# Kernel tuning notes

Hardware: AMD Instinct MI355X
Metric: run time of the kernel (lower is better)

The kernel has to match this reference:

```python
import jax, jax.numpy as jnp
import numpy as np

B, T, C = 2, 2048, 2048
H, HKV, D = 16, 4, 128
THETA = 10000.0
G = H // HKV  # kv groups


def _rope_tables(seq_len, dim, theta):
    inv_freq = 1.0 / theta ** (jnp.arange(0, dim, 2, dtype=jnp.float32) / dim)
    t = jnp.arange(seq_len, dtype=jnp.float32)
    freqs = jnp.outer(t, inv_freq)                 # [T, D/2]
    emb = jnp.concatenate([freqs, freqs], axis=-1)  # [T, D]
    return jnp.cos(emb)[None, None], jnp.sin(emb)[None, None]  # [1,1,T,D]


def _rotate_half(x):
    x1, x2 = jnp.split(x, 2, axis=-1)
    return jnp.concatenate([-x2, x1], axis=-1)


def setup_inputs() -> dict:
    key = jax.random.key(0)
    ks = jax.random.split(key, 6)
    x = jax.random.normal(ks[0], (B, T, C), dtype=jnp.float32)
    s = 0.02
    Wq = jax.random.normal(ks[1], (C, H * D), dtype=jnp.float32) * s
    Wk = jax.random.normal(ks[2], (C, HKV * D), dtype=jnp.float32) * s
    Wv = jax.random.normal(ks[3], (C, HKV * D), dtype=jnp.float32) * s
    Wo = jax.random.normal(ks[4], (H * D, C), dtype=jnp.float32) * s
    mask = jnp.tril(jnp.ones((T, T), dtype=jnp.int32))[None, None]  # causal [1,1,T,T]
    return {"x": x, "Wq": Wq, "Wk": Wk, "Wv": Wv, "Wo": Wo, "mask": mask}


def reference(x, Wq, Wk, Wv, Wo, mask):
    b, t, _ = x.shape
    q = (x @ Wq).reshape(b, t, H, D).transpose(0, 2, 1, 3)      # [B,H,T,D]
    k = (x @ Wk).reshape(b, t, HKV, D).transpose(0, 2, 1, 3)    # [B,HKV,T,D]
    v = (x @ Wv).reshape(b, t, HKV, D).transpose(0, 2, 1, 3)
    cos, sin = _rope_tables(t, D, THETA)
    q = q * cos + _rotate_half(q) * sin
    k = k * cos + _rotate_half(k) * sin
    # expand kv heads (repeat_interleave over head axis)
    k = jnp.repeat(k, G, axis=1)                                # [B,H,T,D]
    v = jnp.repeat(v, G, axis=1)
    attn = jnp.einsum('bhqd,bhkd->bhqk', q, k) / jnp.sqrt(jnp.float32(D))
    attn = jnp.where(mask == 0, jnp.float32(-jnp.inf), attn)
    attn = jax.nn.softmax(attn, axis=-1)
    out = jnp.einsum('bhqk,bhkd->bhqd', attn, v)                # [B,H,T,D]
    out = out.transpose(0, 2, 1, 3).reshape(b, t, H * D)
    return out @ Wo
```

## Files before the change

kernel.cpp:

```cpp
#include <hip/hip_runtime.h>
#include <math.h>

#define B_ 2
#define T_ 2048
#define C_ 2048
#define H_ 16
#define HKV_ 4
#define D_ 128
#define G_ (H_ / HKV_)
#define GK 2048

typedef float f32x4 __attribute__((ext_vector_type(4)));
typedef __bf16 bf16x8 __attribute__((ext_vector_type(8)));

static __device__ __forceinline__ f32x4 mfma16(bf16x8 a, bf16x8 b, f32x4 c) {
    return __builtin_amdgcn_mfma_f32_16x16x32_bf16(a, b, c, 0, 0, 0);
}

static __device__ __forceinline__ void gload16(const __bf16* g, __bf16* l) {
    __builtin_amdgcn_global_load_lds(
        (const __attribute__((address_space(1))) unsigned int*)g,
        (__attribute__((address_space(3))) unsigned int*)l,
        16, 0, 0);
}

__global__ __launch_bounds__(256)
void conv_f32_bf16(const float* __restrict__ src, __bf16* __restrict__ dst, int n8)
{
    const int i = blockIdx.x * blockDim.x + threadIdx.x;
    if (i >= n8) return;
    const float4 a = *(const float4*)&src[(size_t)i * 8];
    const float4 b = *(const float4*)&src[(size_t)i * 8 + 4];
    bf16x8 o;
    o[0] = (__bf16)a.x; o[1] = (__bf16)a.y; o[2] = (__bf16)a.z; o[3] = (__bf16)a.w;
    o[4] = (__bf16)b.x; o[5] = (__bf16)b.y; o[6] = (__bf16)b.z; o[7] = (__bf16)b.w;
    *(bf16x8*)&dst[(size_t)i * 8] = o;
}

__global__ __launch_bounds__(256)
void tconv(const float* __restrict__ src, __bf16* __restrict__ dst, int N)
{
    __shared__ __bf16 tl[32][34];
    const int tx = threadIdx.x;
    const int ty = threadIdx.y;
    const int k0 = blockIdx.x * 32;
    const int n0 = blockIdx.y * 32;

    #pragma unroll
    for (int i = 0; i < 4; ++i) {
        const int r = ty + i * 8;
        tl[r][tx] = (__bf16)src[(size_t)(k0 + r) * N + n0 + tx];
    }
    __syncthreads();
    #pragma unroll
    for (int i = 0; i < 4; ++i) {
        const int r = ty + i * 8;
        dst[(size_t)(n0 + r) * GK + k0 + tx] = tl[tx][r];
    }
}

#define GEMM_MAIN(At, Bt)                                                       \
    __shared__ __bf16 As[128 * 64];                                             \
    __shared__ __bf16 Bs[128 * 64];                                             \
    const int tid = threadIdx.x;                                                \
    const int wave = tid >> 6, lane = tid & 63;                                 \
    const int a = lane & 15, bq = lane >> 4;                                    \
    const int wr = wave >> 1, wc = wave & 1;                                    \
    const int srow = wave * 32 + (lane >> 3);                        \
    const int scol = (lane & 7) * 8;                                            \
    f32x4 acc[4][4];                                                            \
    _Pragma("unroll")                                                           \
    for (int mi = 0; mi < 4; ++mi)                                              \
        _Pragma("unroll")                                                       \
        for (int ni = 0; ni < 4; ++ni) acc[mi][ni] = (f32x4){0.f,0.f,0.f,0.f};  \
    for (int k0 = 0; k0 < GK; k0 += 64) {                                       \
        __syncthreads();                       \
        _Pragma("unroll")                                                       \
        for (int i = 0; i < 4; ++i) {                                           \
            gload16(&(At)[(size_t)(srow + i * 8) * GK + k0 + scol],             \
                    &As[(wave * 32 + i * 8) * 64]);                             \
            gload16(&(Bt)[(size_t)(srow + i * 8) * GK + k0 + scol],             \
                    &Bs[(wave * 32 + i * 8) * 64]);                             \
        }                                                                       \
        __syncthreads();                \
        _Pragma("unroll")                                                       \
        for (int ks = 0; ks < 2; ++ks) {                                        \
            bf16x8 af[4], bfr[4];                                               \
            _Pragma("unroll")                                                   \
            for (int mi = 0; mi < 4; ++mi)                                      \
                af[mi] = *(const bf16x8*)&As[(wr*64 + mi*16 + a) * 64 + ks*32 + bq*8]; \
            _Pragma("unroll")                                                   \
            for (int ni = 0; ni < 4; ++ni)                                      \
                bfr[ni] = *(const bf16x8*)&Bs[(wc*64 + ni*16 + a) * 64 + ks*32 + bq*8]; \
            _Pragma("unroll")                                                   \
            for (int mi = 0; mi < 4; ++mi)                                      \
                _Pragma("unroll")                                               \
                for (int ni = 0; ni < 4; ++ni)                                  \
                    acc[mi][ni] = mfma16(af[mi], bfr[ni], acc[mi][ni]);         \
        }                                                                       \
    }

__global__ __launch_bounds__(256)
void gemm_qkv_mfma(const __bf16* __restrict__ xb,
                   const __bf16* __restrict__ wqt,
                   const __bf16* __restrict__ wkt,
                   const __bf16* __restrict__ wvt,
                   __bf16* __restrict__ qbuf,
                   __bf16* __restrict__ kbuf,
                   __bf16* __restrict__ vbuf)
{
    const int n0 = blockIdx.x * 128;
    const int m0 = blockIdx.y * 128;
    const __bf16* Btp; __bf16* outb; int NH, nloc;
    if (n0 < 2048)      { Btp = wqt + (size_t)n0 * GK;          outb = qbuf; NH = 16; nloc = n0; }
    else if (n0 < 2560) { Btp = wkt + (size_t)(n0 - 2048) * GK; outb = kbuf; NH = 4;  nloc = n0 - 2048; }
    else                { Btp = wvt + (size_t)(n0 - 2560) * GK; outb = vbuf; NH = 4;  nloc = n0 - 2560; }
    const __bf16* Atp = xb + (size_t)m0 * GK;

    GEMM_MAIN(Atp, Btp)

    const int b  = m0 >> 11;
    const int t0 = m0 & (T_ - 1);
    const int h0 = nloc >> 7;
    __bf16* op = outb + (size_t)(b * NH + h0) * T_ * D_;
    #pragma unroll
    for (int mi = 0; mi < 4; ++mi)
        #pragma unroll
        for (int ni = 0; ni < 4; ++ni)
            #pragma unroll
            for (int rr = 0; rr < 4; ++rr) {
                const int row = t0 + wr * 64 + mi * 16 + bq * 4 + rr;
                const int col = wc * 64 + ni * 16 + a;
                op[(size_t)row * D_ + col] = (__bf16)acc[mi][ni][rr];
            }
}

__global__ __launch_bounds__(256)
void gemm_out_mfma(const __bf16* __restrict__ ab,
                   const __bf16* __restrict__ wot,
                   float* __restrict__ outp)
{
    const int n0 = blockIdx.x * 128;
    const int m0 = blockIdx.y * 128;
    const __bf16* Atp = ab + (size_t)m0 * GK;
    const __bf16* Btp = wot + (size_t)n0 * GK;

    GEMM_MAIN(Atp, Btp)

    #pragma unroll
    for (int mi = 0; mi < 4; ++mi)
        #pragma unroll
        for (int ni = 0; ni < 4; ++ni)
            #pragma unroll
            for (int rr = 0; rr < 4; ++rr) {
                const int row = m0 + wr * 64 + mi * 16 + bq * 4 + rr;
                const int col = n0 + wc * 64 + ni * 16 + a;
                outp[(size_t)row * C_ + col] = acc[mi][ni][rr];
            }
}

__global__ void rope_bf16(__bf16* __restrict__ buf)
{
    const int idx = blockIdx.x * blockDim.x + threadIdx.x;
    const int jj  = idx & 31;
    const int row = idx >> 5;
    const int t   = row & (T_ - 1);
    const int d   = jj * 2;

    const float LOG_THETA = 9.210340371976184f;
    const float f1 = (float)t * __expf(-(float)d       * (LOG_THETA / 64.0f));
    const float f2 = (float)t * __expf(-(float)(d + 1) * (LOG_THETA / 64.0f));
    float s1, c1, s2, c2;
    __sincosf(f1, &s1, &c1);
    __sincosf(f2, &s2, &c2);

    __bf16* p = buf + (size_t)row * D_ + d;
    const float x1a = (float)p[0],  x1b = (float)p[1];
    const float x2a = (float)p[64], x2b = (float)p[65];
    p[0]  = (__bf16)(x1a * c1 - x2a * s1);
    p[1]  = (__bf16)(x1b * c2 - x2b * s2);
    p[64] = (__bf16)(x2a * c1 + x1a * s1);
    p[65] = (__bf16)(x2b * c2 + x1b * s2);
}

__global__ __launch_bounds__(256)
void transpose_v(const __bf16* __restrict__ vb, __bf16* __restrict__ vtb)
{
    __shared__ __bf16 tl[32][33];
    const int tx = threadIdx.x;
    const int ty = threadIdx.y;
    const int t0 = blockIdx.x * 32;
    const int d0 = blockIdx.y * 32;
    const int bh = blockIdx.z;

    const __bf16* src = vb + ((size_t)bh * T_ + t0) * D_ + d0;
    #pragma unroll
    for (int i = 0; i < 4; ++i) {
        const int r = ty + i * 8;
        tl[r][tx] = src[(size_t)r * D_ + tx];
    }
    __syncthreads();
    __bf16* dst = vtb + ((size_t)bh * D_ + d0) * T_ + t0;
    #pragma unroll
    for (int i = 0; i < 4; ++i) {
        const int dl = ty + i * 8;
        dst[(size_t)dl * T_ + tx] = tl[tx][dl];
    }
}

#define KS_STRIDE 136
#define VS_STRIDE 36
#define PS_STRIDE 76

__global__ __launch_bounds__(512)
void flash_attn_mfma(const __bf16* __restrict__ qb,
                     const __bf16* __restrict__ kb,
                     const __bf16* __restrict__ vtb,
                     __bf16* __restrict__ abuf)
{
    __shared__ __bf16 KsL[64 * KS_STRIDE];
    __shared__ __bf16 VsL[2 * 128 * VS_STRIDE];
    __shared__ __bf16 PsL[8 * 16 * PS_STRIDE];

    const int tid  = threadIdx.x;
    const int wave = tid >> 6;
    const int lane = tid & 63;
    const int a    = lane & 15;
    const int bq   = lane >> 4;

    const int pair = blockIdx.x;
    const int bh   = blockIdx.y;
    const int b    = bh >> 4;
    const int h    = bh & 15;
    const int kvh  = h >> 2;

    const __bf16* kg  = kb  + (size_t)(b * HKV_ + kvh) * T_ * D_;
    const __bf16* vtg = vtb + (size_t)(b * HKV_ + kvh) * D_ * T_;

    const float scale2 = 0.12750176129424902f;

    for (int half = 0; half < 2; ++half) {
        const int qti = half == 0 ? (15 - pair) : pair;
        const int qt0 = qti * 128;
        const int ntiles = 2 * qti + 2;
        const int qrow_lo = qt0 + wave * 16;

        const __bf16* qg = qb + ((size_t)(b * H_ + h) * T_ + qrow_lo) * D_;
        bf16x8 qf[4];
        #pragma unroll
        for (int ks = 0; ks < 4; ++ks)
            qf[ks] = *(const bf16x8*)&qg[(size_t)a * D_ + ks * 32 + bq * 8];

        f32x4 oacc[8];
        #pragma unroll
        for (int dt = 0; dt < 8; ++dt) oacc[dt] = (f32x4){0.f, 0.f, 0.f, 0.f};
        float m_r[4] = {-INFINITY, -INFINITY, -INFINITY, -INFINITY};
        float l_r[4] = {0.f, 0.f, 0.f, 0.f};

        bf16x8 kpre[2], vpre[2];
        #pragma unroll
        for (int it = 0; it < 2; ++it) {
            const int idx = it * 512 + tid;
            const int r = idx >> 4, c8 = (idx & 15) * 8;
            kpre[it] = *(const bf16x8*)&kg[(size_t)r * D_ + c8];
            const int bo = idx & 3, dd = (idx >> 2) & 127, ss2 = idx >> 9;
            vpre[it] = *(const bf16x8*)&vtg[(size_t)dd * T_ + ss2 * 32 + bo * 8];
        }
        __syncthreads();
        #pragma unroll
        for (int it = 0; it < 2; ++it) {
            const int idx = it * 512 + tid;
            const int r = idx >> 4, c8 = (idx & 15) * 8;
            *(bf16x8*)&KsL[r * KS_STRIDE + c8] = kpre[it];
            const int bo = idx & 3, dd = (idx >> 2) & 127, ss2 = idx >> 9;
            *(bf16x8*)&VsL[(ss2 * 128 + dd) * VS_STRIDE + bo * 8] = vpre[it];
        }
        __syncthreads();

        for (int kt = 0; kt < ntiles; ++kt) {
            const int k0 = kt * 64;
            if (kt + 1 < ntiles) {
                const int k0n = k0 + 64;
                #pragma unroll
                for (int it = 0; it < 2; ++it) {
                    const int idx = it * 512 + tid;
                    const int r = idx >> 4, c8 = (idx & 15) * 8;
                    kpre[it] = *(const bf16x8*)&kg[(size_t)(k0n + r) * D_ + c8];
                    const int bo = idx & 3, dd = (idx >> 2) & 127, ss2 = idx >> 9;
                    vpre[it] = *(const bf16x8*)&vtg[(size_t)dd * T_ + k0n + ss2 * 32 + bo * 8];
                }
            }

            if (k0 <= qrow_lo + 15) {
                f32x4 sacc[4];
                #pragma unroll
                for (int nt = 0; nt < 4; ++nt) {
                    sacc[nt] = (f32x4){0.f, 0.f, 0.f, 0.f};
                    #pragma unroll
                    for (int ks = 0; ks < 4; ++ks) {
                        bf16x8 kf = *(const bf16x8*)&KsL[(nt * 16 + a) * KS_STRIDE + ks * 32 + bq * 8];
                        sacc[nt] = mfma16(qf[ks], kf, sacc[nt]);
                    }
                }

                float p[4][4];
                float mrow[4] = {-INFINITY, -INFINITY, -INFINITY, -INFINITY};
                const bool needmask = (k0 + 63 > qrow_lo);
                #pragma unroll
                for (int nt = 0; nt < 4; ++nt) {
                    const int kc = k0 + nt * 16 + a;
                    #pragma unroll
                    for (int r = 0; r < 4; ++r) {
                        float s = sacc[nt][r] * scale2;
                        if (needmask) {
                            const int qrow = qrow_lo + bq * 4 + r;
                            s = (kc <= qrow) ? s : -INFINITY;
                        }
                        p[nt][r] = s;
                        mrow[r] = fmaxf(mrow[r], s);
                    }
                }
                #pragma unroll
                for (int off = 1; off < 16; off <<= 1)
                    #pragma unroll
                    for (int r = 0; r < 4; ++r)
                        mrow[r] = fmaxf(mrow[r], __shfl_xor(mrow[r], off));

                float corr[4], psum[4];
                #pragma unroll
                for (int r = 0; r < 4; ++r) {
                    const float mnew = fmaxf(m_r[r], mrow[r]);
                    corr[r] = exp2f(m_r[r] - mnew);
                    m_r[r] = mnew;
                    psum[r] = 0.f;
                    #pragma unroll
                    for (int nt = 0; nt < 4; ++nt) {
                        const float pe = exp2f(p[nt][r] - mnew);
                        p[nt][r] = pe;
                        psum[r] += pe;
                    }
                }
                #pragma unroll
                for (int off = 1; off < 16; off <<= 1)
                    #pragma unroll
                    for (int r = 0; r < 4; ++r)
                        psum[r] += __shfl_xor(psum[r], off);
                #pragma unroll
                for (int r = 0; r < 4; ++r) l_r[r] = l_r[r] * corr[r] + psum[r];

                #pragma unroll
                for (int dt = 0; dt < 8; ++dt)
                    #pragma unroll
                    for (int r = 0; r < 4; ++r) oacc[dt][r] *= corr[r];

                #pragma unroll
                for (int nt = 0; nt < 4; ++nt)
                    #pragma unroll
                    for (int r = 0; r < 4; ++r)
                        PsL[(wave * 16 + bq * 4 + r) * PS_STRIDE + nt * 16 + a] = (__bf16)p[nt][r];

                bf16x8 pf[2];
                #pragma unroll
                for (int ss = 0; ss < 2; ++ss)
                    pf[ss] = *(const bf16x8*)&PsL[(wave * 16 + a) * PS_STRIDE + ss * 32 + bq * 8];
                #pragma unroll
                for (int dt = 0; dt < 8; ++dt) {
                    #pragma unroll
                    for (int ss = 0; ss < 2; ++ss) {
                        bf16x8 vf = *(const bf16x8*)&VsL[(ss * 128 + dt * 16 + a) * VS_STRIDE + bq * 8];
                        oacc[dt] = mfma16(pf[ss], vf, oacc[dt]);
                    }
                }
            }

            __syncthreads();
            if (kt + 1 < ntiles) {
                #pragma unroll
                for (int it = 0; it < 2; ++it) {
                    const int idx = it * 512 + tid;
                    const int r = idx >> 4, c8 = (idx & 15) * 8;
                    *(bf16x8*)&KsL[r * KS_STRIDE + c8] = kpre[it];
                    const int bo = idx & 3, dd = (idx >> 2) & 127, ss2 = idx >> 9;
                    *(bf16x8*)&VsL[(ss2 * 128 + dd) * VS_STRIDE + bo * 8] = vpre[it];
                }
                __syncthreads();
            }
        }

        float invl[4];
        #pragma unroll
        for (int r = 0; r < 4; ++r) invl[r] = 1.f / l_r[r];
        #pragma unroll
        for (int dt = 0; dt < 8; ++dt)
            #pragma unroll
            for (int r = 0; r < 4; ++r) {
                const int qrow = qrow_lo + bq * 4 + r;
                abuf[((size_t)(b * T_) + qrow) * (H_ * D_) + h * D_ + dt * 16 + a] =
                    (__bf16)(oacc[dt][r] * invl[r]);
            }
    }
}

extern "C" void kernel_launch(void* const* d_in, const int* in_sizes, int n_in,
                              void* d_out, int out_size, void* d_ws, size_t ws_size,
                              hipStream_t stream)
{
    (void)in_sizes; (void)n_in; (void)out_size; (void)ws_size;
    const float* x  = (const float*)d_in[0];
    const float* Wq = (const float*)d_in[1];
    const float* Wk = (const float*)d_in[2];
    const float* Wv = (const float*)d_in[3];
    const float* Wo = (const float*)d_in[4];
    float* out = (float*)d_out;

    __bf16* xb  = (__bf16*)d_ws;
    __bf16* wqt = xb  + (size_t)4096 * 2048;
    __bf16* wkt = wqt + (size_t)2048 * 2048;
    __bf16* wvt = wkt + (size_t)512 * 2048;
    __bf16* wot = wvt + (size_t)512 * 2048;
    __bf16* qb  = wot + (size_t)2048 * 2048;
    __bf16* kb  = qb  + (size_t)B_ * H_   * T_ * D_;
    __bf16* vb  = kb  + (size_t)B_ * HKV_ * T_ * D_;
    __bf16* vtb = vb  + (size_t)B_ * HKV_ * T_ * D_;
    __bf16* ab  = vtb + (size_t)B_ * HKV_ * T_ * D_;

    hipLaunchKernelGGL(conv_f32_bf16, dim3(4096), dim3(256), 0, stream,
                       x, xb, (int)((size_t)B_ * T_ * C_ / 8));
    hipLaunchKernelGGL(tconv, dim3(64, 64), dim3(32, 8), 0, stream, Wq, wqt, 2048);
    hipLaunchKernelGGL(tconv, dim3(64, 16), dim3(32, 8), 0, stream, Wk, wkt, 512);
    hipLaunchKernelGGL(tconv, dim3(64, 16), dim3(32, 8), 0, stream, Wv, wvt, 512);
    hipLaunchKernelGGL(tconv, dim3(64, 64), dim3(32, 8), 0, stream, Wo, wot, 2048);

    hipLaunchKernelGGL(gemm_qkv_mfma, dim3(24, 32), dim3(256), 0, stream,
                       xb, wqt, wkt, wvt, qb, kb, vb);

    hipLaunchKernelGGL(rope_bf16, dim3(B_ * H_ * T_ * 32 / 256), dim3(256), 0, stream, qb);
    hipLaunchKernelGGL(rope_bf16, dim3(B_ * HKV_ * T_ * 32 / 256), dim3(256), 0, stream, kb);

    hipLaunchKernelGGL(transpose_v, dim3(T_ / 32, D_ / 32, B_ * HKV_), dim3(32, 8), 0, stream,
                       vb, vtb);

    hipLaunchKernelGGL(flash_attn_mfma, dim3(8, B_ * H_), dim3(512), 0, stream,
                       qb, kb, vtb, ab);

    hipLaunchKernelGGL(gemm_out_mfma, dim3(16, 32), dim3(256), 0, stream,
                       ab, wot, out);
}
```

Baseline: 386.9 us.

## Replace GEMMs with 256x256-tile, 8-wave, multi-stage pipelined swizzled kernels

Both projection GEMMs move from 128x128 tiles with a single-buffered LDS load and two barriers per k-step to 256x256 tiles on 512 threads. A 9-slot LDS ring with asynchronous global-to-LDS loads is issued between MFMA phases, alongside XOR swizzling to avoid bank conflicts, setprio around MFMAs, and block-index swizzling for L2 locality. The two RoPE launches are merged into one because kb follows qb contiguously. The large tiles give few blocks (192 and 128) on a 256-CU part, which risks leaving CUs idle, and the heavy LDS use limits occupancy to one block per CU.

```diff
diff --git a/kernel.cpp b/kernel.cpp
--- a/kernel.cpp
+++ b/kernel.cpp
@@ -9,6 +9,7 @@
 #define D_ 128
 #define G_ (H_ / HKV_)
 #define GK 2048
+#define NT9 32
 
 typedef float f32x4 __attribute__((ext_vector_type(4)));
 typedef __bf16 bf16x8 __attribute__((ext_vector_type(8)));
@@ -22,6 +23,142 @@
         (const __attribute__((address_space(1))) unsigned int*)g,
         (__attribute__((address_space(3))) unsigned int*)l,
         16, 0, 0);
+}
+
+#define WRAP9(x) ((x) < 9 ? (x) : (x) - 9)
+
+#define STG(SRC, h, kk, slot) {                                                 \
+    _Pragma("unroll")                                                           \
+    for (int j_ = 0; j_ < 2; ++j_) {                                            \
+        const int lr_ = (h) * 128 + wave * 16 + j_ * 8 + (lane >> 3);           \
+        const int sc_ = ((lane & 7) ^ (lane >> 3)) << 3;                        \
+        gload16(&(SRC)[(size_t)lr_ * GK + (kk) + sc_],                          \
+                &sl[slot][(wave * 16 + j_ * 8) * 64]);                          \
+    } }
+
+#define GEMM8_MAIN(At, Bt)                                                      \
+    __shared__ __bf16 sl[9][8192];                                              \
+    const int tid = threadIdx.x;                                                \
+    const int wave = tid >> 6, lane = tid & 63;                                 \
+    const int a = lane & 15, bq = lane >> 4;                                    \
+    const int wr = wave >> 2, wc = wave & 3;                                    \
+    const int xl = (a & 7) << 3;                                                \
+    const int brow = (wc & 1) * 64;                                             \
+    f32x4 acc[8][4];                                                            \
+    _Pragma("unroll")                                                           \
+    for (int mi = 0; mi < 8; ++mi)                                              \
+        _Pragma("unroll")                                                       \
+        for (int ni = 0; ni < 4; ++ni) acc[mi][ni] = (f32x4){0.f,0.f,0.f,0.f};  \
+            \
+    STG(At, 0, 0, 0) STG(At, 1, 0, 1) STG(Bt, 0, 0, 2) STG(Bt, 1, 0, 3)        \
+    STG(At, 0, 64, 4)                                                           \
+    int s0 = 0;                                                                 \
+    _Pragma("unroll 1")                                                         \
+    for (int t = 0; t < NT9; ++t) {                                             \
+        if (t == NT9 - 1) { asm volatile("s_waitcnt vmcnt(0)" ::: "memory"); }  \
+        else              { asm volatile("s_waitcnt vmcnt(2)" ::: "memory"); }  \
+        __builtin_amdgcn_sched_barrier(0);                                      \
+        __builtin_amdgcn_s_barrier();                                           \
+        __builtin_amdgcn_sched_barrier(0);                                      \
+        const int sA = WRAP9(s0 + wr);                                          \
+        const int sB = WRAP9(s0 + 2 + (wc >> 1));                               \
+        bf16x8 bf_[4][2];                                                       \
+        _Pragma("unroll")                                                       \
+        for (int ni = 0; ni < 4; ++ni)                                          \
+            _Pragma("unroll")                                                   \
+            for (int ks = 0; ks < 2; ++ks)                                      \
+                bf_[ni][ks] = *(const bf16x8*)&sl[sB][(brow + ni*16 + a)*64 +   \
+                                                      ((ks*32 + bq*8) ^ xl)];   \
+        _Pragma("unroll")                                                       \
+        for (int p = 0; p < 4; ++p) {                                           \
+            bf16x8 af_[2][2];                                                   \
+            _Pragma("unroll")                                                   \
+            for (int m = 0; m < 2; ++m)                                         \
+                _Pragma("unroll")                                               \
+                for (int ks = 0; ks < 2; ++ks)                                  \
+                    af_[m][ks] = *(const bf16x8*)&sl[sA][((p*2 + m)*16 + a)*64 +\
+                                                         ((ks*32 + bq*8) ^ xl)];\
+            if (p == 0 && t + 1 < NT9) STG(At, 1, (t+1)*64, WRAP9(s0 + 5))      \
+            if (p == 1 && t + 1 < NT9) STG(Bt, 0, (t+1)*64, WRAP9(s0 + 6))      \
+            if (p == 2 && t + 1 < NT9) STG(Bt, 1, (t+1)*64, WRAP9(s0 + 7))      \
+            if (p == 3 && t + 2 < NT9) STG(At, 0, (t+2)*64, WRAP9(s0 + 8))      \
+            __builtin_amdgcn_s_setprio(1);                                      \
+            _Pragma("unroll")                                                   \
+            for (int m = 0; m < 2; ++m)                                         \
+                _Pragma("unroll")                                               \
+                for (int ni = 0; ni < 4; ++ni) {                                \
+                    acc[p*2+m][ni] = mfma16(af_[m][0], bf_[ni][0], acc[p*2+m][ni]); \
+                    acc[p*2+m][ni] = mfma16(af_[m][1], bf_[ni][1], acc[p*2+m][ni]); \
+                }                                                               \
+            __builtin_amdgcn_s_setprio(0);                                      \
+            if (p < 3) { __builtin_amdgcn_s_barrier(); }                        \
+        }                                                                       \
+        s0 += 4; if (s0 >= 9) s0 -= 9;                                          \
+    }
+
+__global__ __launch_bounds__(512, 1)
+void gemm_qkv8(const __bf16* __restrict__ xb,
+               const __bf16* __restrict__ wqt,
+               const __bf16* __restrict__ wkt,
+               const __bf16* __restrict__ wvt,
+               __bf16* __restrict__ qbuf,
+               __bf16* __restrict__ kbuf,
+               __bf16* __restrict__ vbuf)
+{
+    const int bid = blockIdx.x;
+    const int swz = (bid & 7) * 24 + (bid >> 3);
+    const int mti = swz / 12, nti = swz % 12;
+    const int m0 = mti * 256, n0 = nti * 256;
+
+    const __bf16* Btp; __bf16* outb; int NH, nloc;
+    if (n0 < 2048)      { Btp = wqt + (size_t)n0 * GK;          outb = qbuf; NH = 16; nloc = n0; }
+    else if (n0 < 2560) { Btp = wkt + (size_t)(n0 - 2048) * GK; outb = kbuf; NH = 4;  nloc = n0 - 2048; }
+    else                { Btp = wvt + (size_t)(n0 - 2560) * GK; outb = vbuf; NH = 4;  nloc = n0 - 2560; }
+    const __bf16* Atp = xb + (size_t)m0 * GK;
+
+    GEMM8_MAIN(Atp, Btp)
+
+    #pragma unroll
+    for (int mi = 0; mi < 8; ++mi)
+        #pragma unroll
+        for (int ni = 0; ni < 4; ++ni) {
+            const int col = nloc + wc * 64 + ni * 16 + a;
+            const int head = col >> 7, d = col & 127;
+            #pragma unroll
+            for (int rr = 0; rr < 4; ++rr) {
+                const int row = m0 + wr * 128 + mi * 16 + bq * 4 + rr;
+                const int b = row >> 11, tt = row & (T_ - 1);
+                outb[(((size_t)(b * NH + head)) * T_ + tt) * D_ + d] =
+                    (__bf16)acc[mi][ni][rr];
+            }
+        }
+}
+
+__global__ __launch_bounds__(512, 1)
+void gemm_out8(const __bf16* __restrict__ ab,
+               const __bf16* __restrict__ wot,
+               float* __restrict__ outp)
+{
+    const int bid = blockIdx.x;
+    const int swz = (bid & 7) * 16 + (bid >> 3);
+    const int mti = swz / 8, nti = swz % 8;
+    const int m0 = mti * 256, n0 = nti * 256;
+    const __bf16* Atp = ab + (size_t)m0 * GK;
+    const __bf16* Btp = wot + (size_t)n0 * GK;
+
+    GEMM8_MAIN(Atp, Btp)
+
+    #pragma unroll
+    for (int mi = 0; mi < 8; ++mi)
+        #pragma unroll
+        for (int ni = 0; ni < 4; ++ni) {
+            const int col = n0 + wc * 64 + ni * 16 + a;
+            #pragma unroll
+            for (int rr = 0; rr < 4; ++rr) {
+                const int row = m0 + wr * 128 + mi * 16 + bq * 4 + rr;
+                outp[(size_t)row * C_ + col] = acc[mi][ni][rr];
+            }
+        }
 }
 
 __global__ __launch_bounds__(256)
@@ -59,106 +196,6 @@
     }
 }
 
-#define GEMM_MAIN(At, Bt)                                                       \
-    __shared__ __bf16 As[128 * 64];                                             \
-    __shared__ __bf16 Bs[128 * 64];                                             \
-    const int tid = threadIdx.x;                                                \
-    const int wave = tid >> 6, lane = tid & 63;                                 \
-    const int a = lane & 15, bq = lane >> 4;                                    \
-    const int wr = wave >> 1, wc = wave & 1;                                    \
-    const int srow = wave * 32 + (lane >> 3);                        \
-    const int scol = (lane & 7) * 8;                                            \
-    f32x4 acc[4][4];                                                            \
-    _Pragma("unroll")                                                           \
-    for (int mi = 0; mi < 4; ++mi)                                              \
-        _Pragma("unroll")                                                       \
-        for (int ni = 0; ni < 4; ++ni) acc[mi][ni] = (f32x4){0.f,0.f,0.f,0.f};  \
-    for (int k0 = 0; k0 < GK; k0 += 64) {                                       \
-        __syncthreads();                       \
-        _Pragma("unroll")                                                       \
-        for (int i = 0; i < 4; ++i) {                                           \
-            gload16(&(At)[(size_t)(srow + i * 8) * GK + k0 + scol],             \
-                    &As[(wave * 32 + i * 8) * 64]);                             \
-            gload16(&(Bt)[(size_t)(srow + i * 8) * GK + k0 + scol],             \
-                    &Bs[(wave * 32 + i * 8) * 64]);                             \
-        }                                                                       \
-        __syncthreads();                \
-        _Pragma("unroll")                                                       \
-        for (int ks = 0; ks < 2; ++ks) {                                        \
-            bf16x8 af[4], bfr[4];                                               \
-            _Pragma("unroll")                                                   \
-            for (int mi = 0; mi < 4; ++mi)                                      \
-                af[mi] = *(const bf16x8*)&As[(wr*64 + mi*16 + a) * 64 + ks*32 + bq*8]; \
-            _Pragma("unroll")                                                   \
-            for (int ni = 0; ni < 4; ++ni)                                      \
-                bfr[ni] = *(const bf16x8*)&Bs[(wc*64 + ni*16 + a) * 64 + ks*32 + bq*8]; \
-            _Pragma("unroll")                                                   \
-            for (int mi = 0; mi < 4; ++mi)                                      \
-                _Pragma("unroll")                                               \
-                for (int ni = 0; ni < 4; ++ni)                                  \
-                    acc[mi][ni] = mfma16(af[mi], bfr[ni], acc[mi][ni]);         \
-        }                                                                       \
-    }
-
-__global__ __launch_bounds__(256)
-void gemm_qkv_mfma(const __bf16* __restrict__ xb,
-                   const __bf16* __restrict__ wqt,
-                   const __bf16* __restrict__ wkt,
-                   const __bf16* __restrict__ wvt,
-                   __bf16* __restrict__ qbuf,
-                   __bf16* __restrict__ kbuf,
-                   __bf16* __restrict__ vbuf)
-{
-    const int n0 = blockIdx.x * 128;
-    const int m0 = blockIdx.y * 128;
-    const __bf16* Btp; __bf16* outb; int NH, nloc;
-    if (n0 < 2048)      { Btp = wqt + (size_t)n0 * GK;          outb = qbuf; NH = 16; nloc = n0; }
-    else if (n0 < 2560) { Btp = wkt + (size_t)(n0 - 2048) * GK; outb = kbuf; NH = 4;  nloc = n0 - 2048; }
-    else                { Btp = wvt + (size_t)(n0 - 2560) * GK; outb = vbuf; NH = 4;  nloc = n0 - 2560; }
-    const __bf16* Atp = xb + (size_t)m0 * GK;
-
-    GEMM_MAIN(Atp, Btp)
-
-    const int b  = m0 >> 11;
-    const int t0 = m0 & (T_ - 1);
-    const int h0 = nloc >> 7;
-    __bf16* op = outb + (size_t)(b * NH + h0) * T_ * D_;
-    #pragma unroll
-    for (int mi = 0; mi < 4; ++mi)
-        #pragma unroll
-        for (int ni = 0; ni < 4; ++ni)
-            #pragma unroll
-            for (int rr = 0; rr < 4; ++rr) {
-                const int row = t0 + wr * 64 + mi * 16 + bq * 4 + rr;
-                const int col = wc * 64 + ni * 16 + a;
-                op[(size_t)row * D_ + col] = (__bf16)acc[mi][ni][rr];
-            }
-}
-
-__global__ __launch_bounds__(256)
-void gemm_out_mfma(const __bf16* __restrict__ ab,
-                   const __bf16* __restrict__ wot,
-                   float* __restrict__ outp)
-{
-    const int n0 = blockIdx.x * 128;
-    const int m0 = blockIdx.y * 128;
-    const __bf16* Atp = ab + (size_t)m0 * GK;
-    const __bf16* Btp = wot + (size_t)n0 * GK;
-
-    GEMM_MAIN(Atp, Btp)
-
-    #pragma unroll
-    for (int mi = 0; mi < 4; ++mi)
-        #pragma unroll
-        for (int ni = 0; ni < 4; ++ni)
-            #pragma unroll
-            for (int rr = 0; rr < 4; ++rr) {
-                const int row = m0 + wr * 64 + mi * 16 + bq * 4 + rr;
-                const int col = n0 + wc * 64 + ni * 16 + a;
-                outp[(size_t)row * C_ + col] = acc[mi][ni][rr];
-            }
-}
-
 __global__ void rope_bf16(__bf16* __restrict__ buf)
 {
     const int idx = blockIdx.x * blockDim.x + threadIdx.x;
@@ -311,11 +348,9 @@
                     const int kc = k0 + nt * 16 + a;
                     #pragma unroll
                     for (int r = 0; r < 4; ++r) {
+                        const int qrow = qrow_lo + bq * 4 + r;
                         float s = sacc[nt][r] * scale2;
-                        if (needmask) {
-                            const int qrow = qrow_lo + bq * 4 + r;
-                            s = (kc <= qrow) ? s : -INFINITY;
-                        }
+                        if (needmask) s = (kc <= qrow) ? s : -INFINITY;
                         p[nt][r] = s;
                         mrow[r] = fmaxf(mrow[r], s);
                     }
@@ -431,11 +466,11 @@
     hipLaunchKernelGGL(tconv, dim3(64, 16), dim3(32, 8), 0, stream, Wv, wvt, 512);
     hipLaunchKernelGGL(tconv, dim3(64, 64), dim3(32, 8), 0, stream, Wo, wot, 2048);
 
-    hipLaunchKernelGGL(gemm_qkv_mfma, dim3(24, 32), dim3(256), 0, stream,
+    hipLaunchKernelGGL(gemm_qkv8, dim3(192), dim3(512), 0, stream,
                        xb, wqt, wkt, wvt, qb, kb, vb);
 
-    hipLaunchKernelGGL(rope_bf16, dim3(B_ * H_ * T_ * 32 / 256), dim3(256), 0, stream, qb);
-    hipLaunchKernelGGL(rope_bf16, dim3(B_ * HKV_ * T_ * 32 / 256), dim3(256), 0, stream, kb);
+    hipLaunchKernelGGL(rope_bf16, dim3(B_ * (H_ + HKV_) * T_ * 32 / 256), dim3(256),
+                       0, stream, qb);
 
     hipLaunchKernelGGL(transpose_v, dim3(T_ / 32, D_ / 32, B_ * HKV_), dim3(32, 8), 0, stream,
                        vb, vtb);
@@ -443,6 +478,6 @@
     hipLaunchKernelGGL(flash_attn_mfma, dim3(8, B_ * H_), dim3(512), 0, stream,
                        qb, kb, vtb, ab);
 
-    hipLaunchKernelGGL(gemm_out_mfma, dim3(16, 32), dim3(256), 0, stream,
+    hipLaunchKernelGGL(gemm_out8, dim3(128), dim3(512), 0, stream,
                        ab, wot, out);
 }
```

Result: faster. 355.7 us (-8.1%).
